# Performance work log

Hardware: AMD Instinct MI355X
Metric: run time of the kernel (lower is better)

Reference implementation:

```python
import jax, jax.numpy as jnp
import numpy as np

N = 50000      # total nodes (25 graphs x 2000 proteins)
E = 1200000    # total edges
G = 25         # graphs
F_IN = 128     # protein_features
H = 64         # hidden_dim
L = 2          # num_layers


def setup_inputs() -> dict:
    key = jax.random.key(0)
    ks = jax.random.split(key, 24)
    inp = {
        "x": jax.random.normal(ks[0], (N, F_IN), dtype=jnp.float32),
        "edge_attr": jax.random.uniform(ks[1], (E,), dtype=jnp.float32),
        "global_features": jax.random.normal(ks[2], (G, 6), dtype=jnp.float32),
        "edge_index": jax.random.randint(ks[3], (2, E), 0, N, dtype=jnp.int64),
        "batch": (jnp.arange(N, dtype=jnp.int64) // (N // G)),
    }
    s = 0.05
    inp["W_embed"] = jax.random.normal(ks[4], (F_IN, H), dtype=jnp.float32) * s
    inp["b_embed"] = jnp.zeros((H,), dtype=jnp.float32)
    inp["W_glob"] = jax.random.normal(ks[5], (6, H), dtype=jnp.float32) * s
    inp["b_glob"] = jnp.zeros((H,), dtype=jnp.float32)
    # stacked per-layer GATConv params (heads=1)
    inp["lin_W"] = jax.random.normal(ks[6], (L, H, H), dtype=jnp.float32) * s
    inp["att_src"] = jax.random.normal(ks[7], (L, H), dtype=jnp.float32) * s
    inp["att_dst"] = jax.random.normal(ks[8], (L, H), dtype=jnp.float32) * s
    inp["lin_edge_W"] = jax.random.normal(ks[9], (L, 1, H), dtype=jnp.float32) * s
    inp["att_edge"] = jax.random.normal(ks[10], (L, H), dtype=jnp.float32) * s
    inp["gat_bias"] = jnp.zeros((L, H), dtype=jnp.float32)
    inp["W_comb"] = jax.random.normal(ks[11], (2 * H, H), dtype=jnp.float32) * s
    inp["b_comb"] = jnp.zeros((H,), dtype=jnp.float32)
    inp["W_out"] = jax.random.normal(ks[12], (H, 1), dtype=jnp.float32) * s
    inp["b_out"] = jnp.zeros((1,), dtype=jnp.float32)
    return inp


def _forward(x, edge_attr, global_features, W_embed, b_embed, W_glob, b_glob,
             lin_W, att_src, att_dst, lin_edge_W, att_edge, gat_bias,
             W_comb, b_comb, W_out, b_out, edge_index, batch):
    src, dst = edge_index[0], edge_index[1]
    h = x @ W_embed + b_embed                       # [N,H]
    g = global_features @ W_glob + b_glob           # [G,H]
    ea = edge_attr[:, None]                         # [E,1] (edge_attr.unsqueeze(1))
    for l in range(L):
        hs = h @ lin_W[l]                           # [N,H] shared lin_src/lin_dst
        a_src = hs @ att_src[l]                     # [N]
        a_dst = hs @ att_dst[l]                     # [N]
        ef = ea @ lin_edge_W[l]                     # [E,H]
        a_edge = ef @ att_edge[l]                   # [E]
        alpha = jax.nn.leaky_relu(a_src[src] + a_dst[dst] + a_edge, 0.2)
        # segment softmax over incoming edges of each dst node
        m = jax.ops.segment_max(alpha, dst, num_segments=N)
        ex = jnp.exp(alpha - m[dst])
        denom = jax.ops.segment_sum(ex, dst, num_segments=N)
        alpha = ex / (denom[dst] + 1e-16)
        msg = alpha[:, None] * hs[src]              # [E,H]
        h = jax.ops.segment_sum(msg, dst, num_segments=N) + gat_bias[l]
        h = jax.nn.relu(h)
    # global_mean_pool
    counts = jax.ops.segment_sum(jnp.ones((N,), h.dtype), batch, num_segments=G)
    graph = jax.ops.segment_sum(h, batch, num_segments=G) / counts[:, None]
    combined = jax.nn.relu(jnp.concatenate([graph, g], axis=1) @ W_comb + b_comb)
    return combined @ W_out + b_out                 # [G,1]


def reference(x, edge_attr, global_features, W_embed, b_embed, W_glob, b_glob,
              lin_W, att_src, att_dst, lin_edge_W, att_edge, gat_bias,
              W_comb, b_comb, W_out, b_out, edge_index, batch):
    return _forward(x, edge_attr, global_features, W_embed, b_embed, W_glob, b_glob,
                    lin_W, att_src, att_dst, lin_edge_W, att_edge, gat_bias,
                    W_comb, b_comb, W_out, b_out, edge_index, batch)
```

## Files before the change

kernel.cpp:

```cpp
#include <hip/hip_runtime.h>
#include <math.h>

#define N_NODES 50000
#define N_EDGES 1200000
#define N_GRAPH 25
#define F_IN 128
#define H_DIM 64
#define NODES_PER_GRAPH 2000
#define POOL_CHUNKS 32

#define NBUCK 196
#define BUCK_CAP 8000
#define EPB 4096
#define NB_BIN ((N_EDGES + EPB - 1) / EPB)
#define NB_GEMM ((N_NODES + 63) / 64)

#define OFF_H     0
#define OFF_HS    (N_NODES*64)
#define OFF_ASRC  (OFF_HS + N_NODES*64)
#define OFF_ADST  (OFF_ASRC + N_NODES)
#define OFF_CBUF  (OFF_ADST + N_NODES)
#define OFF_ZERO  (OFF_CBUF + 16)
#define OFF_BCUR  OFF_ZERO
#define OFF_GSUM  (OFF_BCUR + 256)
#define OFF_ZEND  (OFF_GSUM + N_GRAPH*64)
#define OFF_BBASE OFF_ZEND
#define OFF_ROWP  (OFF_BBASE + 256)
#define OFF_ESRT  (OFF_ROWP + N_NODES + 2)

__global__ __launch_bounds__(256) void k_embed(const float* __restrict__ x,
                                               const float* __restrict__ W,
                                               const float* __restrict__ b,
                                               float* __restrict__ h) {
    __shared__ float4 sW4[F_IN * 16];
    __shared__ float4 sx4[64 * 17];
    int tid = threadIdx.x;
    int n0 = blockIdx.x * 64;
    const float4* W4 = (const float4*)W;
    const float4* x4 = (const float4*)x;
    #pragma unroll
    for (int i = 0; i < 8; ++i) sW4[tid + i * 256] = W4[tid + i * 256];

    int c4 = tid & 15, ng = tid >> 4;
    int r = tid >> 4, q = tid & 15;
    float4 acc[4];
    #pragma unroll
    for (int j = 0; j < 4; ++j) acc[j] = make_float4(0.f, 0.f, 0.f, 0.f);

    for (int kh = 0; kh < 2; ++kh) {
        __syncthreads();
        #pragma unroll
        for (int rb = 0; rb < 4; ++rb) {
            int rr = r + rb * 16;
            int n = n0 + rr;
            float4 v = make_float4(0.f, 0.f, 0.f, 0.f);
            if (n < N_NODES) v = x4[(size_t)n * 32 + kh * 16 + q];
            sx4[rr * 17 + q] = v;
        }
        __syncthreads();
        #pragma unroll
        for (int kq = 0; kq < 16; ++kq) {
            float4 wv[4];
            #pragma unroll
            for (int kk = 0; kk < 4; ++kk) wv[kk] = sW4[(kh * 64 + kq * 4 + kk) * 16 + c4];
            #pragma unroll
            for (int j = 0; j < 4; ++j) {
                float4 xv = sx4[(ng * 4 + j) * 17 + kq];
                float xs[4] = {xv.x, xv.y, xv.z, xv.w};
                #pragma unroll
                for (int kk = 0; kk < 4; ++kk) {
                    acc[j].x = fmaf(xs[kk], wv[kk].x, acc[j].x);
                    acc[j].y = fmaf(xs[kk], wv[kk].y, acc[j].y);
                    acc[j].z = fmaf(xs[kk], wv[kk].z, acc[j].z);
                    acc[j].w = fmaf(xs[kk], wv[kk].w, acc[j].w);
                }
            }
        }
    }
    float4 bb = ((const float4*)b)[c4];
    #pragma unroll
    for (int j = 0; j < 4; ++j) {
        int n = n0 + ng * 4 + j;
        if (n < N_NODES) {
            float4 v;
            v.x = acc[j].x + bb.x; v.y = acc[j].y + bb.y;
            v.z = acc[j].z + bb.z; v.w = acc[j].w + bb.w;
            ((float4*)h)[(size_t)n * 16 + c4] = v;
        }
    }
}

__global__ __launch_bounds__(256) void k_hs(const float* __restrict__ hin,
                                            const float* __restrict__ W,
                                            const float* __restrict__ attS,
                                            const float* __restrict__ attD,
                                            float* __restrict__ hs,
                                            float* __restrict__ asrc,
                                            float* __restrict__ adst) {
    __shared__ float4 sW4[H_DIM * 16];
    __shared__ float4 sx4[64 * 17];
    int tid = threadIdx.x;
    int n0 = blockIdx.x * 64;
    const float4* W4 = (const float4*)W;
    const float4* h4 = (const float4*)hin;
    #pragma unroll
    for (int i = 0; i < 4; ++i) sW4[tid + i * 256] = W4[tid + i * 256];
    int r = tid >> 4, q = tid & 15;
    #pragma unroll
    for (int rb = 0; rb < 4; ++rb) {
        int rr = r + rb * 16;
        int n = n0 + rr;
        float4 v = make_float4(0.f, 0.f, 0.f, 0.f);
        if (n < N_NODES) v = h4[(size_t)n * 16 + q];
        sx4[rr * 17 + q] = v;
    }
    __syncthreads();

    int c4 = tid & 15, ng = tid >> 4;
    float4 acc[4];
    #pragma unroll
    for (int j = 0; j < 4; ++j) acc[j] = make_float4(0.f, 0.f, 0.f, 0.f);
    #pragma unroll
    for (int kq = 0; kq < 16; ++kq) {
        float4 wv[4];
        #pragma unroll
        for (int kk = 0; kk < 4; ++kk) wv[kk] = sW4[(kq * 4 + kk) * 16 + c4];
        #pragma unroll
        for (int j = 0; j < 4; ++j) {
            float4 xv = sx4[(ng * 4 + j) * 17 + kq];
            float xs[4] = {xv.x, xv.y, xv.z, xv.w};
            #pragma unroll
            for (int kk = 0; kk < 4; ++kk) {
                acc[j].x = fmaf(xs[kk], wv[kk].x, acc[j].x);
                acc[j].y = fmaf(xs[kk], wv[kk].y, acc[j].y);
                acc[j].z = fmaf(xs[kk], wv[kk].z, acc[j].z);
                acc[j].w = fmaf(xs[kk], wv[kk].w, acc[j].w);
            }
        }
    }
    float4 aS = ((const float4*)attS)[c4];
    float4 aD = ((const float4*)attD)[c4];
    #pragma unroll
    for (int j = 0; j < 4; ++j) {
        int n = n0 + ng * 4 + j;
        float rs = acc[j].x * aS.x + acc[j].y * aS.y + acc[j].z * aS.z + acc[j].w * aS.w;
        float rd = acc[j].x * aD.x + acc[j].y * aD.y + acc[j].z * aD.z + acc[j].w * aD.w;
        #pragma unroll
        for (int o = 1; o < 16; o <<= 1) {
            rs += __shfl_xor(rs, o);
            rd += __shfl_xor(rd, o);
        }
        if (n < N_NODES) {
            ((float4*)hs)[(size_t)n * 16 + c4] = acc[j];
            if (c4 == 0) { asrc[n] = rs; adst[n] = rd; }
        }
    }
}

__device__ __forceinline__ int block_excl_scan(int v, int tid, int* lds, int* total) {
    int lane = tid & 63, w = tid >> 6;
    int incl = v;
    #pragma unroll
    for (int off = 1; off < 64; off <<= 1) {
        int t = __shfl_up(incl, off);
        if (lane >= off) incl += t;
    }
    if (lane == 63) lds[w] = incl;
    __syncthreads();
    int wo = 0;
    for (int i = 0; i < w; ++i) wo += lds[i];
    *total = lds[0] + lds[1] + lds[2] + lds[3];
    __syncthreads();
    return wo + incl - v;
}

__global__ __launch_bounds__(256) void k_bin(const int* __restrict__ ei,
                                             const float* __restrict__ ea,
                                             uint2* __restrict__ stage,
                                             int* __restrict__ bcur) {
    __shared__ int lcnt[NBUCK];
    __shared__ int lbase[NBUCK];
    int tid = threadIdx.x;
    for (int i = tid; i < NBUCK; i += 256) lcnt[i] = 0;
    __syncthreads();
    int e0 = blockIdx.x * EPB;
    unsigned pw0[16], pw1[16];
    #pragma unroll
    for (int k = 0; k < 16; ++k) {
        int e = e0 + k * 256 + tid;
        bool ok = e < N_EDGES;
        int s = ok ? ei[e] : 0;
        int d = ok ? ei[N_EDGES + e] : 0;
        float v = ok ? ea[e] : 0.f;
        pw0[k] = (unsigned)s | ((unsigned)d << 16);
        pw1[k] = __float_as_uint(v);
        if (ok) atomicAdd(&lcnt[d >> 8], 1);
    }
    __syncthreads();
    for (int i = tid; i < NBUCK; i += 256) {
        lbase[i] = atomicAdd(&bcur[i], lcnt[i]);
        lcnt[i] = 0;
    }
    __syncthreads();
    #pragma unroll
    for (int k = 0; k < 16; ++k) {
        int e = e0 + k * 256 + tid;
        if (e < N_EDGES) {
            int b = pw0[k] >> 24;
            int pos = lbase[b] + atomicAdd(&lcnt[b], 1);
            uint2 t; t.x = pw0[k]; t.y = pw1[k];
            stage[b * BUCK_CAP + pos] = t;
        }
    }
}

__global__ __launch_bounds__(256) void k_bscan(const int* __restrict__ bcur,
                                               int* __restrict__ bbase,
                                               int* __restrict__ rowp,
                                               const float* __restrict__ linE,
                                               const float* __restrict__ attE,
                                               float* __restrict__ cbuf) {
    __shared__ int lds[4];
    if (threadIdx.x < 128) {
        int l = threadIdx.x >> 6, j = threadIdx.x & 63;
        float v = linE[l * 64 + j] * attE[l * 64 + j];
        #pragma unroll
        for (int m = 1; m < 64; m <<= 1) v += __shfl_xor(v, m);
        if (j == 0) cbuf[l] = v;
    }
    int v = (threadIdx.x < NBUCK) ? bcur[threadIdx.x] : 0;
    int total;
    int ex = block_excl_scan(v, threadIdx.x, lds, &total);
    if (threadIdx.x < NBUCK) bbase[threadIdx.x] = ex;
    if (threadIdx.x == 0) rowp[N_NODES] = N_EDGES;
}

__global__ __launch_bounds__(256) void k_group(const uint2* __restrict__ stage,
                                               const int* __restrict__ bcur,
                                               const int* __restrict__ bbase,
                                               int* __restrict__ rowp,
                                               unsigned* __restrict__ esrt) {
    int b = blockIdx.x;
    int tid = threadIdx.x;
    int cntb = bcur[b];
    int base = bbase[b];
    __shared__ int lcnt[256];
    __shared__ int lofs[256];
    __shared__ int slds[4];
    lcnt[tid] = 0;
    __syncthreads();
    const uint2* reg = stage + b * BUCK_CAP;
    for (int i = tid; i < cntb; i += 256)
        atomicAdd(&lcnt[(reg[i].x >> 16) & 255], 1);
    __syncthreads();
    int total;
    int ex = block_excl_scan(lcnt[tid], tid, slds, &total);
    lofs[tid] = base + ex;
    int n = b * 256 + tid;
    if (n < N_NODES) rowp[n] = base + ex;
    __syncthreads();
    lcnt[tid] = 0;
    __syncthreads();
    for (int i = tid; i < cntb; i += 256) {
        uint2 v = reg[i];
        int dloc = (v.x >> 16) & 255;
        int pos = lofs[dloc] + atomicAdd(&lcnt[dloc], 1);
        esrt[pos] = (v.x & 0xFFFFu) | ((v.y + 0x8000u) & 0xFFFF0000u);
    }
}

__global__ __launch_bounds__(256) void k_fused(const int* __restrict__ rowp,
                                               const unsigned* __restrict__ esrt,
                                               const float* __restrict__ asrc,
                                               const float* __restrict__ adst,
                                               const float* __restrict__ hs,
                                               const float* __restrict__ cbuf,
                                               int layer,
                                               const float* __restrict__ gbias,
                                               float* __restrict__ hout) {
    int wid = (blockIdx.x * 256 + threadIdx.x) >> 6;
    int lane = threadIdx.x & 63;
    if (wid >= N_NODES) return;
    int beg = rowp[wid], end = rowp[wid + 1];
    float adv = adst[wid];
    float c = cbuf[layer];
    float m = -INFINITY, sum = 0.f;
    float4 acc = make_float4(0.f, 0.f, 0.f, 0.f);
    int g = lane >> 4, fl = lane & 15;
    const float4* hs4 = (const float4*)hs;

    for (int base = beg; base < end; base += 64) {
        int idx = base + lane;
        bool ok = idx < end;
        unsigned v = ok ? esrt[idx] : 0u;
        int s = v & 0xFFFF;
        float a;
        if (ok) {
            float eav = __uint_as_float(v & 0xFFFF0000u);
            a = asrc[s] + adv + c * eav;
            a = a >= 0.f ? a : 0.2f * a;
        } else {
            a = -INFINITY;
        }
        float cm = a;
        #pragma unroll
        for (int o = 1; o < 64; o <<= 1) cm = fmaxf(cm, __shfl_xor(cm, o));
        float newm = fmaxf(m, cm);
        float scale = __expf(m - newm);
        sum *= scale;
        acc.x *= scale; acc.y *= scale; acc.z *= scale; acc.w *= scale;
        m = newm;
        float ex = ok ? __expf(a - m) : 0.f;
        float cs = ex;
        #pragma unroll
        for (int o = 1; o < 64; o <<= 1) cs += __shfl_xor(cs, o);
        sum += cs;

        int lim = end - base; if (lim > 64) lim = 64;
        int t = g;
        for (; t + 12 < lim; t += 16) {
            float w0 = __shfl(ex, t),      w1 = __shfl(ex, t + 4);
            float w2 = __shfl(ex, t + 8),  w3 = __shfl(ex, t + 12);
            int   s0 = __shfl(s, t),       s1 = __shfl(s, t + 4);
            int   s2 = __shfl(s, t + 8),   s3 = __shfl(s, t + 12);
            float4 r0 = hs4[s0 * 16 + fl];
            float4 r1 = hs4[s1 * 16 + fl];
            float4 r2 = hs4[s2 * 16 + fl];
            float4 r3 = hs4[s3 * 16 + fl];
            acc.x += w0 * r0.x; acc.y += w0 * r0.y; acc.z += w0 * r0.z; acc.w += w0 * r0.w;
            acc.x += w1 * r1.x; acc.y += w1 * r1.y; acc.z += w1 * r1.z; acc.w += w1 * r1.w;
            acc.x += w2 * r2.x; acc.y += w2 * r2.y; acc.z += w2 * r2.z; acc.w += w2 * r2.w;
            acc.x += w3 * r3.x; acc.y += w3 * r3.y; acc.z += w3 * r3.z; acc.w += w3 * r3.w;
        }
        for (; t < lim; t += 4) {
            float w0 = __shfl(ex, t);
            int   s0 = __shfl(s, t);
            float4 r0 = hs4[s0 * 16 + fl];
            acc.x += w0 * r0.x; acc.y += w0 * r0.y; acc.z += w0 * r0.z; acc.w += w0 * r0.w;
        }
    }
    acc.x += __shfl_xor(acc.x, 16); acc.y += __shfl_xor(acc.y, 16);
    acc.z += __shfl_xor(acc.z, 16); acc.w += __shfl_xor(acc.w, 16);
    acc.x += __shfl_xor(acc.x, 32); acc.y += __shfl_xor(acc.y, 32);
    acc.z += __shfl_xor(acc.z, 32); acc.w += __shfl_xor(acc.w, 32);

    if (lane < 16) {
        float inv = 1.f / (sum + 1e-16f);
        float4 gb = ((const float4*)(gbias + layer * H_DIM))[lane];
        float4 val;
        val.x = acc.x * inv + gb.x; val.x = val.x > 0.f ? val.x : 0.f;
        val.y = acc.y * inv + gb.y; val.y = val.y > 0.f ? val.y : 0.f;
        val.z = acc.z * inv + gb.z; val.z = val.z > 0.f ? val.z : 0.f;
        val.w = acc.w * inv + gb.w; val.w = val.w > 0.f ? val.w : 0.f;
        ((float4*)(hout + (size_t)wid * H_DIM))[lane] = val;
    }
}

__global__ __launch_bounds__(256) void k_pool(const float* __restrict__ h,
                                              float* __restrict__ gsum) {
    int g = blockIdx.x / POOL_CHUNKS;
    int chunk = blockIdx.x % POOL_CHUNKS;
    int wave = threadIdx.x >> 6, lane = threadIdx.x & 63;
    const int per_chunk = (NODES_PER_GRAPH + POOL_CHUNKS - 1) / POOL_CHUNKS;
    int n0 = g * NODES_PER_GRAPH + chunk * per_chunk;
    int n1 = g * NODES_PER_GRAPH + min((chunk + 1) * per_chunk, NODES_PER_GRAPH);
    float sum = 0.f;
    for (int n = n0 + wave; n < n1; n += 4)
        sum += h[(size_t)n * H_DIM + lane];
    __shared__ float spart[4][64];
    spart[wave][lane] = sum;
    __syncthreads();
    if (wave == 0) {
        float tot = spart[0][lane] + spart[1][lane] + spart[2][lane] + spart[3][lane];
        atomicAdd(gsum + g * H_DIM + lane, tot);
    }
}

__global__ __launch_bounds__(64) void k_head2(const float* __restrict__ gsum,
                                              const float* __restrict__ gf,
                                              const float* __restrict__ Wg,
                                              const float* __restrict__ bg,
                                              const float* __restrict__ Wc,
                                              const float* __restrict__ bc,
                                              const float* __restrict__ Wo,
                                              const float* __restrict__ bo,
                                              float* __restrict__ out) {
    int g = blockIdx.x;
    int lane = threadIdx.x;
    __shared__ float sgraph[64];
    __shared__ float sgf[64];
    sgraph[lane] = gsum[g * H_DIM + lane] / (float)NODES_PER_GRAPH;
    float gv = bg[lane];
    #pragma unroll
    for (int k = 0; k < 6; ++k) gv += gf[g * 6 + k] * Wg[k * 64 + lane];
    sgf[lane] = gv;
    __syncthreads();
    float cj = bc[lane];
    #pragma unroll
    for (int k = 0; k < 64; ++k) cj += sgraph[k] * Wc[k * 64 + lane];
    #pragma unroll
    for (int k = 0; k < 64; ++k) cj += sgf[k] * Wc[(64 + k) * 64 + lane];
    cj = cj > 0.f ? cj : 0.f;
    float o = cj * Wo[lane];
    #pragma unroll
    for (int m = 1; m < 64; m <<= 1) o += __shfl_xor(o, m);
    if (lane == 0) out[g] = o + bo[0];
}

extern "C" void kernel_launch(void* const* d_in, const int* in_sizes, int n_in,
                              void* d_out, int out_size, void* d_ws, size_t ws_size,
                              hipStream_t stream) {
    const float* x        = (const float*)d_in[0];
    const float* ea       = (const float*)d_in[1];
    const float* gf       = (const float*)d_in[2];
    const int*   ei       = (const int*)d_in[3];
    const float* W_embed  = (const float*)d_in[5];
    const float* b_embed  = (const float*)d_in[6];
    const float* W_glob   = (const float*)d_in[7];
    const float* b_glob   = (const float*)d_in[8];
    const float* lin_W    = (const float*)d_in[9];
    const float* att_src  = (const float*)d_in[10];
    const float* att_dst  = (const float*)d_in[11];
    const float* lin_eW   = (const float*)d_in[12];
    const float* att_edge = (const float*)d_in[13];
    const float* gat_bias = (const float*)d_in[14];
    const float* W_comb   = (const float*)d_in[15];
    const float* b_comb   = (const float*)d_in[16];
    const float* W_out    = (const float*)d_in[17];
    const float* b_out    = (const float*)d_in[18];
    float* out = (float*)d_out;
    float* ws  = (float*)d_ws;

    float*    h      = ws + OFF_H;
    float*    hs     = ws + OFF_HS;
    uint2*    stage  = (uint2*)(ws + OFF_HS);
    float*    asrc   = ws + OFF_ASRC;
    float*    adst   = ws + OFF_ADST;
    float*    cbuf   = ws + OFF_CBUF;
    int*      bcur   = (int*)(ws + OFF_BCUR);
    float*    gsum   = ws + OFF_GSUM;
    int*      bbase  = (int*)(ws + OFF_BBASE);
    int*      rowp   = (int*)(ws + OFF_ROWP);
    unsigned* esrt   = (unsigned*)(ws + OFF_ESRT);

    hipMemsetAsync(ws + OFF_ZERO, 0, (size_t)(OFF_ZEND - OFF_ZERO) * sizeof(float), stream);
    k_embed<<<NB_GEMM, 256, 0, stream>>>(x, W_embed, b_embed, h);

    k_bin<<<NB_BIN, 256, 0, stream>>>(ei, ea, stage, bcur);
    k_bscan<<<1, 256, 0, stream>>>(bcur, bbase, rowp, lin_eW, att_edge, cbuf);
    k_group<<<NBUCK, 256, 0, stream>>>(stage, bcur, bbase, rowp, esrt);

    for (int l = 0; l < 2; ++l) {
        k_hs<<<NB_GEMM, 256, 0, stream>>>(h, lin_W + l * 64 * 64,
                                          att_src + l * 64, att_dst + l * 64,
                                          hs, asrc, adst);
        k_fused<<<(N_NODES + 3) / 4, 256, 0, stream>>>(rowp, esrt,
                                                       asrc, adst, hs, cbuf, l,
                                                       gat_bias, h);
    }

    k_pool<<<N_GRAPH * POOL_CHUNKS, 256, 0, stream>>>(h, gsum);
    k_head2<<<N_GRAPH, 64, 0, stream>>>(gsum, gf, W_glob, b_glob,
                                        W_comb, b_comb, W_out, b_out, out);
}
```

Before: 215.8 us.

## Store projected node features as fp16 and fold setup kernels into neighbors

The projected features hs are written as packed fp16, and the aggregation kernel gathers 16-byte fp16 rows, with 8 lanes per edge instead of 16, accumulating in fp32. This halves the bytes of the random neighbor gathers that dominate aggregation. The memset and the single-block bucket-scan kernel are removed: zeroing and the cbuf computation move into block 0 of the embed kernel, and every group block recomputes the bucket prefix scan itself. The fp16 storage adds rounding error to the messages, and block 0 of the embed kernel does extra work.

```diff
diff --git a/kernel.cpp b/kernel.cpp
--- a/kernel.cpp
+++ b/kernel.cpp
@@ -1,4 +1,5 @@
 #include <hip/hip_runtime.h>
+#include <hip/hip_fp16.h>
 #include <math.h>
 
 #define N_NODES 50000
@@ -20,21 +21,34 @@
 #define OFF_ASRC  (OFF_HS + N_NODES*64)
 #define OFF_ADST  (OFF_ASRC + N_NODES)
 #define OFF_CBUF  (OFF_ADST + N_NODES)
-#define OFF_ZERO  (OFF_CBUF + 16)
-#define OFF_BCUR  OFF_ZERO
+#define OFF_BCUR  (OFF_CBUF + 16)
 #define OFF_GSUM  (OFF_BCUR + 256)
-#define OFF_ZEND  (OFF_GSUM + N_GRAPH*64)
-#define OFF_BBASE OFF_ZEND
-#define OFF_ROWP  (OFF_BBASE + 256)
+#define OFF_ROWP  (OFF_GSUM + N_GRAPH*64)
 #define OFF_ESRT  (OFF_ROWP + N_NODES + 2)
 
 __global__ __launch_bounds__(256) void k_embed(const float* __restrict__ x,
                                                const float* __restrict__ W,
                                                const float* __restrict__ b,
-                                               float* __restrict__ h) {
+                                               float* __restrict__ h,
+                                               const float* __restrict__ linE,
+                                               const float* __restrict__ attE,
+                                               float* __restrict__ cbuf,
+                                               int* __restrict__ bcur,
+                                               float* __restrict__ gsum) {
     __shared__ float4 sW4[F_IN * 16];
     __shared__ float4 sx4[64 * 17];
     int tid = threadIdx.x;
+    if (blockIdx.x == 0) {
+        for (int i = tid; i < 256; i += 256) bcur[i] = 0;
+        for (int i = tid; i < N_GRAPH * 64; i += 256) gsum[i] = 0.f;
+        if (tid < 128) {
+            int l = tid >> 6, j = tid & 63;
+            float v = linE[l * 64 + j] * attE[l * 64 + j];
+            #pragma unroll
+            for (int m = 1; m < 64; m <<= 1) v += __shfl_xor(v, m);
+            if (j == 0) cbuf[l] = v;
+        }
+    }
     int n0 = blockIdx.x * 64;
     const float4* W4 = (const float4*)W;
     const float4* x4 = (const float4*)x;
@@ -94,7 +108,7 @@
                                             const float* __restrict__ W,
                                             const float* __restrict__ attS,
                                             const float* __restrict__ attD,
-                                            float* __restrict__ hs,
+                                            __half* __restrict__ hs_h,
                                             float* __restrict__ asrc,
                                             float* __restrict__ adst) {
     __shared__ float4 sW4[H_DIM * 16];
@@ -151,7 +165,12 @@
             rd += __shfl_xor(rd, o);
         }
         if (n < N_NODES) {
-            ((float4*)hs)[(size_t)n * 16 + c4] = acc[j];
+            __half2 p0 = __floats2half2_rn(acc[j].x, acc[j].y);
+            __half2 p1 = __floats2half2_rn(acc[j].z, acc[j].w);
+            uint2 st;
+            st.x = *(unsigned*)&p0;
+            st.y = *(unsigned*)&p1;
+            ((uint2*)hs_h)[(size_t)n * 16 + c4] = st;
             if (c4 == 0) { asrc[n] = rs; adst[n] = rd; }
         }
     }
@@ -214,50 +233,33 @@
     }
 }
 
-__global__ __launch_bounds__(256) void k_bscan(const int* __restrict__ bcur,
-                                               int* __restrict__ bbase,
-                                               int* __restrict__ rowp,
-                                               const float* __restrict__ linE,
-                                               const float* __restrict__ attE,
-                                               float* __restrict__ cbuf) {
-    __shared__ int lds[4];
-    if (threadIdx.x < 128) {
-        int l = threadIdx.x >> 6, j = threadIdx.x & 63;
-        float v = linE[l * 64 + j] * attE[l * 64 + j];
-        #pragma unroll
-        for (int m = 1; m < 64; m <<= 1) v += __shfl_xor(v, m);
-        if (j == 0) cbuf[l] = v;
-    }
-    int v = (threadIdx.x < NBUCK) ? bcur[threadIdx.x] : 0;
-    int total;
-    int ex = block_excl_scan(v, threadIdx.x, lds, &total);
-    if (threadIdx.x < NBUCK) bbase[threadIdx.x] = ex;
-    if (threadIdx.x == 0) rowp[N_NODES] = N_EDGES;
-}
-
 __global__ __launch_bounds__(256) void k_group(const uint2* __restrict__ stage,
                                                const int* __restrict__ bcur,
-                                               const int* __restrict__ bbase,
                                                int* __restrict__ rowp,
                                                unsigned* __restrict__ esrt) {
     int b = blockIdx.x;
     int tid = threadIdx.x;
-    int cntb = bcur[b];
-    int base = bbase[b];
+    __shared__ int sprefix[256];
     __shared__ int lcnt[256];
     __shared__ int lofs[256];
     __shared__ int slds[4];
+    int bv = (tid < NBUCK) ? bcur[tid] : 0;
+    int total;
+    int bex = block_excl_scan(bv, tid, slds, &total);
+    sprefix[tid] = bex;
     lcnt[tid] = 0;
     __syncthreads();
+    int base = sprefix[b];
+    int cntb = bcur[b];
     const uint2* reg = stage + b * BUCK_CAP;
     for (int i = tid; i < cntb; i += 256)
         atomicAdd(&lcnt[(reg[i].x >> 16) & 255], 1);
     __syncthreads();
-    int total;
     int ex = block_excl_scan(lcnt[tid], tid, slds, &total);
     lofs[tid] = base + ex;
     int n = b * 256 + tid;
     if (n < N_NODES) rowp[n] = base + ex;
+    if (b == 0 && tid == 0) rowp[N_NODES] = N_EDGES;
     __syncthreads();
     lcnt[tid] = 0;
     __syncthreads();
@@ -273,7 +275,7 @@
                                                const unsigned* __restrict__ esrt,
                                                const float* __restrict__ asrc,
                                                const float* __restrict__ adst,
-                                               const float* __restrict__ hs,
+                                               const __half* __restrict__ hs_h,
                                                const float* __restrict__ cbuf,
                                                int layer,
                                                const float* __restrict__ gbias,
@@ -285,9 +287,23 @@
     float adv = adst[wid];
     float c = cbuf[layer];
     float m = -INFINITY, sum = 0.f;
-    float4 acc = make_float4(0.f, 0.f, 0.f, 0.f);
-    int g = lane >> 4, fl = lane & 15;
-    const float4* hs4 = (const float4*)hs;
+    float acc[8];
+    #pragma unroll
+    for (int j = 0; j < 8; ++j) acc[j] = 0.f;
+    int g8 = lane >> 3, fl8 = lane & 7;
+    const uint4* hsq = (const uint4*)hs_h;
+
+#define UNPACK_FMA(w_, r_)                                                      \
+    {                                                                           \
+        __half2 h0_ = *(__half2*)&r_.x, h1_ = *(__half2*)&r_.y;                 \
+        __half2 h2_ = *(__half2*)&r_.z, h3_ = *(__half2*)&r_.w;                 \
+        float2 f0_ = __half22float2(h0_), f1_ = __half22float2(h1_);            \
+        float2 f2_ = __half22float2(h2_), f3_ = __half22float2(h3_);            \
+        acc[0] = fmaf(w_, f0_.x, acc[0]); acc[1] = fmaf(w_, f0_.y, acc[1]);     \
+        acc[2] = fmaf(w_, f1_.x, acc[2]); acc[3] = fmaf(w_, f1_.y, acc[3]);     \
+        acc[4] = fmaf(w_, f2_.x, acc[4]); acc[5] = fmaf(w_, f2_.y, acc[5]);     \
+        acc[6] = fmaf(w_, f3_.x, acc[6]); acc[7] = fmaf(w_, f3_.y, acc[7]);     \
+    }
 
     for (int base = beg; base < end; base += 64) {
         int idx = base + lane;
@@ -308,7 +324,8 @@
         float newm = fmaxf(m, cm);
         float scale = __expf(m - newm);
         sum *= scale;
-        acc.x *= scale; acc.y *= scale; acc.z *= scale; acc.w *= scale;
+        #pragma unroll
+        for (int j = 0; j < 8; ++j) acc[j] *= scale;
         m = newm;
         float ex = ok ? __expf(a - m) : 0.f;
         float cs = ex;
@@ -317,42 +334,50 @@
         sum += cs;
 
         int lim = end - base; if (lim > 64) lim = 64;
-        int t = g;
-        for (; t + 12 < lim; t += 16) {
-            float w0 = __shfl(ex, t),      w1 = __shfl(ex, t + 4);
-            float w2 = __shfl(ex, t + 8),  w3 = __shfl(ex, t + 12);
-            int   s0 = __shfl(s, t),       s1 = __shfl(s, t + 4);
-            int   s2 = __shfl(s, t + 8),   s3 = __shfl(s, t + 12);
-            float4 r0 = hs4[s0 * 16 + fl];
-            float4 r1 = hs4[s1 * 16 + fl];
-            float4 r2 = hs4[s2 * 16 + fl];
-            float4 r3 = hs4[s3 * 16 + fl];
-            acc.x += w0 * r0.x; acc.y += w0 * r0.y; acc.z += w0 * r0.z; acc.w += w0 * r0.w;
-            acc.x += w1 * r1.x; acc.y += w1 * r1.y; acc.z += w1 * r1.z; acc.w += w1 * r1.w;
-            acc.x += w2 * r2.x; acc.y += w2 * r2.y; acc.z += w2 * r2.z; acc.w += w2 * r2.w;
-            acc.x += w3 * r3.x; acc.y += w3 * r3.y; acc.z += w3 * r3.z; acc.w += w3 * r3.w;
-        }
-        for (; t < lim; t += 4) {
+        int t = g8;
+        for (; t + 24 < lim; t += 32) {
+            float w0 = __shfl(ex, t),      w1 = __shfl(ex, t + 8);
+            float w2 = __shfl(ex, t + 16), w3 = __shfl(ex, t + 24);
+            int   s0 = __shfl(s, t),       s1 = __shfl(s, t + 8);
+            int   s2 = __shfl(s, t + 16),  s3 = __shfl(s, t + 24);
+            uint4 r0 = hsq[s0 * 8 + fl8];
+            uint4 r1 = hsq[s1 * 8 + fl8];
+            uint4 r2 = hsq[s2 * 8 + fl8];
+            uint4 r3 = hsq[s3 * 8 + fl8];
+            UNPACK_FMA(w0, r0);
+            UNPACK_FMA(w1, r1);
+            UNPACK_FMA(w2, r2);
+            UNPACK_FMA(w3, r3);
+        }
+        for (; t < lim; t += 8) {
             float w0 = __shfl(ex, t);
             int   s0 = __shfl(s, t);
-            float4 r0 = hs4[s0 * 16 + fl];
-            acc.x += w0 * r0.x; acc.y += w0 * r0.y; acc.z += w0 * r0.z; acc.w += w0 * r0.w;
-        }
-    }
-    acc.x += __shfl_xor(acc.x, 16); acc.y += __shfl_xor(acc.y, 16);
-    acc.z += __shfl_xor(acc.z, 16); acc.w += __shfl_xor(acc.w, 16);
-    acc.x += __shfl_xor(acc.x, 32); acc.y += __shfl_xor(acc.y, 32);
-    acc.z += __shfl_xor(acc.z, 32); acc.w += __shfl_xor(acc.w, 32);
-
-    if (lane < 16) {
+            uint4 r0 = hsq[s0 * 8 + fl8];
+            UNPACK_FMA(w0, r0);
+        }
+    }
+#undef UNPACK_FMA
+    #pragma unroll
+    for (int o = 8; o < 64; o <<= 1) {
+        #pragma unroll
+        for (int j = 0; j < 8; ++j) acc[j] += __shfl_xor(acc[j], o);
+    }
+
+    if (lane < 8) {
         float inv = 1.f / (sum + 1e-16f);
-        float4 gb = ((const float4*)(gbias + layer * H_DIM))[lane];
-        float4 val;
-        val.x = acc.x * inv + gb.x; val.x = val.x > 0.f ? val.x : 0.f;
-        val.y = acc.y * inv + gb.y; val.y = val.y > 0.f ? val.y : 0.f;
-        val.z = acc.z * inv + gb.z; val.z = val.z > 0.f ? val.z : 0.f;
-        val.w = acc.w * inv + gb.w; val.w = val.w > 0.f ? val.w : 0.f;
-        ((float4*)(hout + (size_t)wid * H_DIM))[lane] = val;
+        const float* gb = gbias + layer * H_DIM + lane * 8;
+        float* op = hout + (size_t)wid * H_DIM + lane * 8;
+        float4 v0, v1;
+        v0.x = acc[0] * inv + gb[0]; v0.x = v0.x > 0.f ? v0.x : 0.f;
+        v0.y = acc[1] * inv + gb[1]; v0.y = v0.y > 0.f ? v0.y : 0.f;
+        v0.z = acc[2] * inv + gb[2]; v0.z = v0.z > 0.f ? v0.z : 0.f;
+        v0.w = acc[3] * inv + gb[3]; v0.w = v0.w > 0.f ? v0.w : 0.f;
+        v1.x = acc[4] * inv + gb[4]; v1.x = v1.x > 0.f ? v1.x : 0.f;
+        v1.y = acc[5] * inv + gb[5]; v1.y = v1.y > 0.f ? v1.y : 0.f;
+        v1.z = acc[6] * inv + gb[6]; v1.z = v1.z > 0.f ? v1.z : 0.f;
+        v1.w = acc[7] * inv + gb[7]; v1.w = v1.w > 0.f ? v1.w : 0.f;
+        ((float4*)op)[0] = v0;
+        ((float4*)op)[1] = v1;
     }
 }
 
@@ -432,30 +457,28 @@
     float* ws  = (float*)d_ws;
 
     float*    h      = ws + OFF_H;
-    float*    hs     = ws + OFF_HS;
+    __half*   hs_h   = (__half*)(ws + OFF_HS);
     uint2*    stage  = (uint2*)(ws + OFF_HS);
     float*    asrc   = ws + OFF_ASRC;
     float*    adst   = ws + OFF_ADST;
     float*    cbuf   = ws + OFF_CBUF;
     int*      bcur   = (int*)(ws + OFF_BCUR);
     float*    gsum   = ws + OFF_GSUM;
-    int*      bbase  = (int*)(ws + OFF_BBASE);
     int*      rowp   = (int*)(ws + OFF_ROWP);
     unsigned* esrt   = (unsigned*)(ws + OFF_ESRT);
 
-    hipMemsetAsync(ws + OFF_ZERO, 0, (size_t)(OFF_ZEND - OFF_ZERO) * sizeof(float), stream);
-    k_embed<<<NB_GEMM, 256, 0, stream>>>(x, W_embed, b_embed, h);
+    k_embed<<<NB_GEMM, 256, 0, stream>>>(x, W_embed, b_embed, h,
+                                         lin_eW, att_edge, cbuf, bcur, gsum);
 
     k_bin<<<NB_BIN, 256, 0, stream>>>(ei, ea, stage, bcur);
-    k_bscan<<<1, 256, 0, stream>>>(bcur, bbase, rowp, lin_eW, att_edge, cbuf);
-    k_group<<<NBUCK, 256, 0, stream>>>(stage, bcur, bbase, rowp, esrt);
+    k_group<<<NBUCK, 256, 0, stream>>>(stage, bcur, rowp, esrt);
 
     for (int l = 0; l < 2; ++l) {
         k_hs<<<NB_GEMM, 256, 0, stream>>>(h, lin_W + l * 64 * 64,
                                           att_src + l * 64, att_dst + l * 64,
-                                          hs, asrc, adst);
+                                          hs_h, asrc, adst);
         k_fused<<<(N_NODES + 3) / 4, 256, 0, stream>>>(rowp, esrt,
-                                                       asrc, adst, hs, cbuf, l,
+                                                       asrc, adst, hs_h, cbuf, l,
                                                        gat_bias, h);
     }
 
```

Result: faster. 202.7 us (-6.1%).
